# Performance work log

Hardware: AMD Instinct MI355X
Metric: run time of the kernel (lower is better)

Reference implementation:

```python
import jax, jax.numpy as jnp
import numpy as np

H = 12          # num_heads
HS = 64         # head_size
ALL = H * HS    # all_size = 768
P = 128         # max_position_offset


def _rel_pos_ids(S, P):
    # Toeplitz relative-position ids, same as scipy.linalg.toeplitz(c, r)
    r = np.clip(np.arange(S), None, P - 1)
    c = np.clip(-np.arange(S), -P + 1, None)
    c[1:] += 2 * P
    d = np.arange(S)[None, :] - np.arange(S)[:, None]  # j - i
    ids = np.where(d >= 0, r[np.clip(d, 0, None)], c[np.clip(-d, 0, None)])
    return jnp.asarray(ids, jnp.int32)


def setup_inputs() -> dict:
    key = jax.random.key(0)
    ks = jax.random.split(key, 8)
    B, S = 2, 1024
    return {
        "p0": jax.random.normal(ks[0], (1, 1), jnp.float32),
        "p1": jax.random.normal(ks[1], (B, S, ALL), jnp.float32),
        "p2": jax.random.normal(ks[2], (1, 1), jnp.float32),
        "W_qk": jax.random.normal(ks[3], (ALL, 2 * ALL), jnp.float32) * 0.02,
        "b_qk": jnp.zeros((2 * ALL,), jnp.float32),
        "rel_emb": jax.random.normal(ks[4], (2 * P + 2, HS), jnp.float32) * 0.02,
        "W_out": jax.random.normal(ks[5], (H, 64), jnp.float32) * 0.1,
        "b_out": jnp.zeros((64,), jnp.float32),
    }


def reference(p0, p1, p2, W_qk, b_qk, rel_emb, W_out, b_out):
    B, S, _ = p1.shape
    scaling = HS ** 0.25  # sqrt(sqrt(head_size))
    # reader[1]: Linear -> concat(query, key)
    u = p1 @ W_qk + b_qk                                        # [B,S,2*ALL]
    q = (u[..., :ALL] / scaling).reshape(B, S, H, HS).transpose(0, 2, 1, 3)  # [B,H,S,HS]
    k = (u[..., ALL:] / scaling).reshape(B, S, H, HS).transpose(0, 2, 1, 3)  # [B,H,S,HS]
    scores = jnp.einsum('bhsd,bhtd->bhst', q, k)                # [B,H,S,S]
    # relative position bias: rpe[s,t,:] . q[b,h,s,:]
    ids = _rel_pos_ids(S, P)                                    # [S,S] int
    rpe = rel_emb[ids] / scaling                                # [S,S,HS]
    bias = jnp.einsum('std,bhsd->bhst', rpe, q)                 # [B,H,S,S]
    out = (scores + bias).transpose(0, 2, 3, 1)                 # [B,S,S,H]
    # writer: Linear(num_heads -> predicate_dims[2])
    return out @ W_out + b_out                                  # [B,S,S,64]
```

## Files before the change

kernel.cpp:

```cpp
#include <hip/hip_runtime.h>
#include <math.h>

#define SEQ   1024
#define BATCH 2
#define NH    12
#define ALLD  768
#define INVS  0.35355339059327373f

typedef __attribute__((ext_vector_type(8)))  __bf16 bf16x8;
typedef __attribute__((ext_vector_type(16))) float  f32x16;
typedef __attribute__((ext_vector_type(2)))  float  f32x2;

__global__ __launch_bounds__(256) void qk_gemm(
    const float* __restrict__ p1, const float* __restrict__ Wqk,
    const float* __restrict__ bqk, __bf16* __restrict__ qf,
    __bf16* __restrict__ kf) {
  const int tid = threadIdx.x;
  const int l = tid & 63, w = tid >> 6;
  const int l31 = l & 31, half = l >> 5;
  const int m0 = blockIdx.x * 64;
  const int mw = (w >> 1) * 32;
  const int nw = blockIdx.y * 64 + (w & 1) * 32;

  __shared__ __bf16 Af[8][66][8];

  f32x16 acc;
#pragma unroll
  for (int e = 0; e < 16; ++e) acc[e] = 0.f;

  const int arow = tid >> 2;
  const int aq = tid & 3;

  for (int kk = 0; kk < 768; kk += 64) {
    __syncthreads();
    {
      const float* ap = p1 + (size_t)(m0 + arow) * 768 + kk + aq * 16;
      float4 a0 = ((const float4*)ap)[0];
      float4 a1 = ((const float4*)ap)[1];
      float4 a2 = ((const float4*)ap)[2];
      float4 a3 = ((const float4*)ap)[3];
      bf16x8 f0, f1;
      f0[0] = (__bf16)a0.x; f0[1] = (__bf16)a0.y;
      f0[2] = (__bf16)a0.z; f0[3] = (__bf16)a0.w;
      f0[4] = (__bf16)a1.x; f0[5] = (__bf16)a1.y;
      f0[6] = (__bf16)a1.z; f0[7] = (__bf16)a1.w;
      f1[0] = (__bf16)a2.x; f1[1] = (__bf16)a2.y;
      f1[2] = (__bf16)a2.z; f1[3] = (__bf16)a2.w;
      f1[4] = (__bf16)a3.x; f1[5] = (__bf16)a3.y;
      f1[6] = (__bf16)a3.z; f1[7] = (__bf16)a3.w;
      *(bf16x8*)&Af[aq * 2 + 0][arow][0] = f0;
      *(bf16x8*)&Af[aq * 2 + 1][arow][0] = f1;
    }
    __syncthreads();
#pragma unroll
    for (int ksl = 0; ksl < 4; ++ksl) {
      const float* bsrc =
          Wqk + (size_t)(kk + ksl * 16 + half * 8) * 1536 + nw + l31;
      bf16x8 bf;
#pragma unroll
      for (int e = 0; e < 8; ++e) bf[e] = (__bf16)bsrc[(size_t)e * 1536];
      bf16x8 af = *(const bf16x8*)&Af[ksl * 2 + half][mw + l31][0];
      acc = __builtin_amdgcn_mfma_f32_32x32x16_bf16(af, bf, acc, 0, 0, 0);
    }
  }

  const int n = nw + l31;
  const float bias = bqk[n];
  const bool is_q = (n < ALLD);
  const int nn = is_q ? n : n - ALLD;
  const int h = nn >> 6, dd = nn & 63;
  const int ks4 = dd >> 4, hf = (dd >> 3) & 1, e = dd & 7;
  __bf16* fdst = is_q ? qf : kf;
#pragma unroll
  for (int r = 0; r < 16; ++r) {
    const int m = m0 + mw + (r & 3) + 8 * (r >> 2) + 4 * half;
    const int bb = m >> 10, ss = m & 1023;
    const float v = (acc[r] + bias) * INVS;
    fdst[((((size_t)(bb * NH + h) * 4 + ks4) * 2 + hf) * SEQ + ss) * 8 + e] =
        (__bf16)v;
  }
}

__global__ __launch_bounds__(256, 4) void main_kernel(
    const __bf16* __restrict__ qf, const __bf16* __restrict__ kf,
    const float* __restrict__ rel, const float* __restrict__ Wout,
    const float* __restrict__ bout, float* __restrict__ out) {
  const int tid = threadIdx.x;
  const int l = tid & 63, w = tid >> 6;
  const int l31 = l & 31, half = l >> 5;

  const int raw = blockIdx.x + (blockIdx.y << 5) + (blockIdx.z << 10);
  const int swz = (raw & 7) * 256 + (raw >> 3);
  const int t0 = (swz & 31) * 32;
  const int s0 = ((swz >> 5) & 31) * 32;
  const int b = swz >> 10;
  const int D = t0 - s0;

  __shared__ __attribute__((aligned(16))) char smem[40960];
  float(*rel_s)[66] = (float(*)[66])smem;
  __bf16(*P)[20] = (__bf16(*)[20])smem;

  {
    const int c = tid >> 2, q = tid & 3;
    const int d = D - 32 + c;
    const int id = (d >= 0) ? (d < 127 ? d : 127) : (d > -127 ? d + 256 : 129);
    const float4* src = (const float4*)(rel + (size_t)id * 64 + q * 16);
    float4* dst = (float4*)&rel_s[c][q * 16];
#pragma unroll
    for (int i = 0; i < 4; ++i) dst[i] = src[i];
  }
  __syncthreads();

  bf16x8 relfrag[4][2];
#pragma unroll
  for (int ks = 0; ks < 4; ++ks) {
#pragma unroll
    for (int cb = 0; cb < 2; ++cb) {
      const int c = cb * 32 + l31;
      const int base = ks * 16 + half * 8;
      float4 r0 = *(const float4*)&rel_s[c][base];
      float4 r1 = *(const float4*)&rel_s[c][base + 4];
      bf16x8 f;
      f[0] = (__bf16)r0.x; f[1] = (__bf16)r0.y;
      f[2] = (__bf16)r0.z; f[3] = (__bf16)r0.w;
      f[4] = (__bf16)r1.x; f[5] = (__bf16)r1.y;
      f[6] = (__bf16)r1.z; f[7] = (__bf16)r1.w;
      relfrag[ks][cb] = f;
    }
  }
  __syncthreads();

  {
    ushort4 z = {0, 0, 0, 0};
#pragma unroll
    for (int i = 0; i < 4; ++i) *(ushort4*)&P[tid * 4 + i][12] = z;
  }

  const bf16x8* qfp = (const bf16x8*)qf;
  const bf16x8* kfp = (const bf16x8*)kf;

#pragma unroll
  for (int hh = 0; hh < 3; ++hh) {
    const int h = w * 3 + hh;
    f32x16 acc, bacc0, bacc1;
#pragma unroll
    for (int e = 0; e < 16; ++e) { acc[e] = 0.f; bacc0[e] = 0.f; bacc1[e] = 0.f; }
#pragma unroll
    for (int ks = 0; ks < 4; ++ks) {
      const size_t pbase = (((size_t)(b * NH + h) * 4 + ks) * 2 + half) * SEQ;
      bf16x8 af = qfp[pbase + s0 + l31];
      bf16x8 bvk = kfp[pbase + t0 + l31];
      acc = __builtin_amdgcn_mfma_f32_32x32x16_bf16(af, bvk, acc, 0, 0, 0);
      bacc0 = __builtin_amdgcn_mfma_f32_32x32x16_bf16(af, relfrag[ks][0],
                                                      bacc0, 0, 0, 0);
      bacc1 = __builtin_amdgcn_mfma_f32_32x32x16_bf16(af, relfrag[ks][1],
                                                      bacc1, 0, 0, 0);
    }
#pragma unroll
    for (int r = 0; r < 16; ++r) {
      const int sl = (r & 3) + 8 * (r >> 2) + 4 * half;
      const int src = (l31 - sl) & 31;
      const float v0 = __shfl(bacc0[r], src, 32);
      const float v1 = __shfl(bacc1[r], src, 32);
      const float bias = (l31 >= sl) ? v1 : v0;
      const float v = acc[r] + bias * INVS;
      P[sl * 32 + l31][h] = (__bf16)v;
    }
  }
  __syncthreads();

  bf16x8 wfrag0, wfrag1;
#pragma unroll
  for (int e = 0; e < 8; ++e) {
    const int hh = half * 8 + e;
    wfrag0[e] = (__bf16)((hh < NH) ? Wout[hh * 64 + 2 * l31] : 0.f);
    wfrag1[e] = (__bf16)((hh < NH) ? Wout[hh * 64 + 2 * l31 + 1] : 0.f);
  }
  const float bo0 = bout[2 * l31];
  const float bo1 = bout[2 * l31 + 1];

  float* obase = out + ((((size_t)b << 10) + s0) << 10) * 64 + (size_t)t0 * 64;
#pragma unroll 1
  for (int rt = w; rt < 32; rt += 4) {
    bf16x8 af = *(const bf16x8*)&P[rt * 32 + l31][half * 8];
    f32x16 o0, o1;
#pragma unroll
    for (int e = 0; e < 16; ++e) { o0[e] = 0.f; o1[e] = 0.f; }
    o0 = __builtin_amdgcn_mfma_f32_32x32x16_bf16(af, wfrag0, o0, 0, 0, 0);
    o1 = __builtin_amdgcn_mfma_f32_32x32x16_bf16(af, wfrag1, o1, 0, 0, 0);
    float* orow = obase + ((size_t)rt << 16) + 2 * l31;
#pragma unroll
    for (int r = 0; r < 16; ++r) {
      const int tl = (r & 3) + 8 * (r >> 2) + 4 * half;
      f32x2 v;
      v.x = o0[r] + bo0;
      v.y = o1[r] + bo1;
      __builtin_nontemporal_store(v, (f32x2*)(orow + ((size_t)tl << 6)));
    }
  }
}

extern "C" void kernel_launch(void* const* d_in, const int* in_sizes, int n_in,
                              void* d_out, int out_size, void* d_ws,
                              size_t ws_size, hipStream_t stream) {
  const float* p1 = (const float*)d_in[1];
  const float* Wqk = (const float*)d_in[3];
  const float* bqk = (const float*)d_in[4];
  const float* rel = (const float*)d_in[5];
  const float* Wout = (const float*)d_in[6];
  const float* bout = (const float*)d_in[7];
  float* out = (float*)d_out;

  __bf16* qf = (__bf16*)d_ws;
  __bf16* kf = qf + 1572864;

  hipLaunchKernelGGL(qk_gemm, dim3(32, 24), dim3(256), 0, stream, p1, Wqk, bqk,
                     qf, kf);
  hipLaunchKernelGGL(main_kernel, dim3(SEQ / 32, SEQ / 32, BATCH), dim3(256),
                     0, stream, qf, kf, rel, Wout, bout, out);
}
```

Baseline: 134.7 us.

## Widen main kernel tile to 32x64 and reuse rel embeddings across two subtiles

Each block of the main kernel now covers 64 key positions (two 32-wide subtiles) instead of 32, halving the grid to 1024 blocks. It loads 96 relative-embedding rows once, so the two subtiles share the middle 32-row fragment and reuse the Q fragments. It also drops the occupancy hint from the launch bounds. This is meant to amortise per-block setup (rel loads, bf16 conversion, W_out fragments). In exchange each block does more serial work, with an extra barrier between the subtiles, and holds more registers.

```diff
diff --git a/kernel.cpp b/kernel.cpp
--- a/kernel.cpp
+++ b/kernel.cpp
@@ -81,7 +81,7 @@
   }
 }
 
-__global__ __launch_bounds__(256, 4) void main_kernel(
+__global__ __launch_bounds__(256) void main_kernel(
     const __bf16* __restrict__ qf, const __bf16* __restrict__ kf,
     const float* __restrict__ rel, const float* __restrict__ Wout,
     const float* __restrict__ bout, float* __restrict__ out) {
@@ -89,33 +89,38 @@
   const int l = tid & 63, w = tid >> 6;
   const int l31 = l & 31, half = l >> 5;
 
-  const int raw = blockIdx.x + (blockIdx.y << 5) + (blockIdx.z << 10);
-  const int swz = (raw & 7) * 256 + (raw >> 3);
-  const int t0 = (swz & 31) * 32;
-  const int s0 = ((swz >> 5) & 31) * 32;
-  const int b = swz >> 10;
+  const int raw = blockIdx.x;
+  const int swz = (raw & 7) * 128 + (raw >> 3);
+  const int t0 = (swz & 15) * 64;
+  const int s0 = ((swz >> 4) & 31) * 32;
+  const int b = swz >> 9;
   const int D = t0 - s0;
 
   __shared__ __attribute__((aligned(16))) char smem[40960];
   float(*rel_s)[66] = (float(*)[66])smem;
   __bf16(*P)[20] = (__bf16(*)[20])smem;
 
-  {
-    const int c = tid >> 2, q = tid & 3;
-    const int d = D - 32 + c;
-    const int id = (d >= 0) ? (d < 127 ? d : 127) : (d > -127 ? d + 256 : 129);
-    const float4* src = (const float4*)(rel + (size_t)id * 64 + q * 16);
-    float4* dst = (float4*)&rel_s[c][q * 16];
-#pragma unroll
-    for (int i = 0; i < 4; ++i) dst[i] = src[i];
+#pragma unroll
+  for (int i = 0; i < 2; ++i) {
+    const int task = tid + 256 * i;
+    if (task < 384) {
+      const int c = task >> 2, q = task & 3;
+      const int d = D - 32 + c;
+      const int id =
+          (d >= 0) ? (d < 127 ? d : 127) : (d > -127 ? d + 256 : 129);
+      const float4* src = (const float4*)(rel + (size_t)id * 64 + q * 16);
+      float4* dst = (float4*)&rel_s[c][q * 16];
+#pragma unroll
+      for (int k = 0; k < 4; ++k) dst[k] = src[k];
+    }
   }
   __syncthreads();
 
-  bf16x8 relfrag[4][2];
+  bf16x8 relfrag[4][3];
 #pragma unroll
   for (int ks = 0; ks < 4; ++ks) {
 #pragma unroll
-    for (int cb = 0; cb < 2; ++cb) {
+    for (int cb = 0; cb < 3; ++cb) {
       const int c = cb * 32 + l31;
       const int base = ks * 16 + half * 8;
       float4 r0 = *(const float4*)&rel_s[c][base];
@@ -136,39 +141,6 @@
     for (int i = 0; i < 4; ++i) *(ushort4*)&P[tid * 4 + i][12] = z;
   }
 
-  const bf16x8* qfp = (const bf16x8*)qf;
-  const bf16x8* kfp = (const bf16x8*)kf;
-
-#pragma unroll
-  for (int hh = 0; hh < 3; ++hh) {
-    const int h = w * 3 + hh;
-    f32x16 acc, bacc0, bacc1;
-#pragma unroll
-    for (int e = 0; e < 16; ++e) { acc[e] = 0.f; bacc0[e] = 0.f; bacc1[e] = 0.f; }
-#pragma unroll
-    for (int ks = 0; ks < 4; ++ks) {
-      const size_t pbase = (((size_t)(b * NH + h) * 4 + ks) * 2 + half) * SEQ;
-      bf16x8 af = qfp[pbase + s0 + l31];
-      bf16x8 bvk = kfp[pbase + t0 + l31];
-      acc = __builtin_amdgcn_mfma_f32_32x32x16_bf16(af, bvk, acc, 0, 0, 0);
-      bacc0 = __builtin_amdgcn_mfma_f32_32x32x16_bf16(af, relfrag[ks][0],
-                                                      bacc0, 0, 0, 0);
-      bacc1 = __builtin_amdgcn_mfma_f32_32x32x16_bf16(af, relfrag[ks][1],
-                                                      bacc1, 0, 0, 0);
-    }
-#pragma unroll
-    for (int r = 0; r < 16; ++r) {
-      const int sl = (r & 3) + 8 * (r >> 2) + 4 * half;
-      const int src = (l31 - sl) & 31;
-      const float v0 = __shfl(bacc0[r], src, 32);
-      const float v1 = __shfl(bacc1[r], src, 32);
-      const float bias = (l31 >= sl) ? v1 : v0;
-      const float v = acc[r] + bias * INVS;
-      P[sl * 32 + l31][h] = (__bf16)v;
-    }
-  }
-  __syncthreads();
-
   bf16x8 wfrag0, wfrag1;
 #pragma unroll
   for (int e = 0; e < 8; ++e) {
@@ -179,24 +151,67 @@
   const float bo0 = bout[2 * l31];
   const float bo1 = bout[2 * l31 + 1];
 
-  float* obase = out + ((((size_t)b << 10) + s0) << 10) * 64 + (size_t)t0 * 64;
+  const bf16x8* qfp = (const bf16x8*)qf;
+  const bf16x8* kfp = (const bf16x8*)kf;
+
 #pragma unroll 1
-  for (int rt = w; rt < 32; rt += 4) {
-    bf16x8 af = *(const bf16x8*)&P[rt * 32 + l31][half * 8];
-    f32x16 o0, o1;
-#pragma unroll
-    for (int e = 0; e < 16; ++e) { o0[e] = 0.f; o1[e] = 0.f; }
-    o0 = __builtin_amdgcn_mfma_f32_32x32x16_bf16(af, wfrag0, o0, 0, 0, 0);
-    o1 = __builtin_amdgcn_mfma_f32_32x32x16_bf16(af, wfrag1, o1, 0, 0, 0);
-    float* orow = obase + ((size_t)rt << 16) + 2 * l31;
-#pragma unroll
-    for (int r = 0; r < 16; ++r) {
-      const int tl = (r & 3) + 8 * (r >> 2) + 4 * half;
-      f32x2 v;
-      v.x = o0[r] + bo0;
-      v.y = o1[r] + bo1;
-      __builtin_nontemporal_store(v, (f32x2*)(orow + ((size_t)tl << 6)));
-    }
+  for (int tt = 0; tt < 2; ++tt) {
+    const int tb = t0 + tt * 32;
+
+#pragma unroll
+    for (int hh = 0; hh < 3; ++hh) {
+      const int h = w * 3 + hh;
+      f32x16 acc, bacc0, bacc1;
+#pragma unroll
+      for (int e = 0; e < 16; ++e) {
+        acc[e] = 0.f; bacc0[e] = 0.f; bacc1[e] = 0.f;
+      }
+#pragma unroll
+      for (int ks = 0; ks < 4; ++ks) {
+        const size_t pbase =
+            (((size_t)(b * NH + h) * 4 + ks) * 2 + half) * SEQ;
+        bf16x8 af = qfp[pbase + s0 + l31];
+        bf16x8 bvk = kfp[pbase + tb + l31];
+        acc = __builtin_amdgcn_mfma_f32_32x32x16_bf16(af, bvk, acc, 0, 0, 0);
+        bacc0 = __builtin_amdgcn_mfma_f32_32x32x16_bf16(af, relfrag[ks][tt],
+                                                        bacc0, 0, 0, 0);
+        bacc1 = __builtin_amdgcn_mfma_f32_32x32x16_bf16(
+            af, relfrag[ks][tt + 1], bacc1, 0, 0, 0);
+      }
+#pragma unroll
+      for (int r = 0; r < 16; ++r) {
+        const int sl = (r & 3) + 8 * (r >> 2) + 4 * half;
+        const int src = (l31 - sl) & 31;
+        const float v0 = __shfl(bacc0[r], src, 32);
+        const float v1 = __shfl(bacc1[r], src, 32);
+        const float bias = (l31 >= sl) ? v1 : v0;
+        const float v = acc[r] + bias * INVS;
+        P[sl * 32 + l31][h] = (__bf16)v;
+      }
+    }
+    __syncthreads();
+
+    float* obase =
+        out + ((((size_t)b << 10) + s0) << 10) * 64 + (size_t)tb * 64;
+#pragma unroll 1
+    for (int rt = w; rt < 32; rt += 4) {
+      bf16x8 af = *(const bf16x8*)&P[rt * 32 + l31][half * 8];
+      f32x16 o0, o1;
+#pragma unroll
+      for (int e = 0; e < 16; ++e) { o0[e] = 0.f; o1[e] = 0.f; }
+      o0 = __builtin_amdgcn_mfma_f32_32x32x16_bf16(af, wfrag0, o0, 0, 0, 0);
+      o1 = __builtin_amdgcn_mfma_f32_32x32x16_bf16(af, wfrag1, o1, 0, 0, 0);
+      float* orow = obase + ((size_t)rt << 16) + 2 * l31;
+#pragma unroll
+      for (int r = 0; r < 16; ++r) {
+        const int tl = (r & 3) + 8 * (r >> 2) + 4 * half;
+        f32x2 v;
+        v.x = o0[r] + bo0;
+        v.y = o1[r] + bo1;
+        __builtin_nontemporal_store(v, (f32x2*)(orow + ((size_t)tl << 6)));
+      }
+    }
+    if (tt == 0) __syncthreads();
   }
 }
 
@@ -216,6 +231,6 @@
 
   hipLaunchKernelGGL(qk_gemm, dim3(32, 24), dim3(256), 0, stream, p1, Wqk, bqk,
                      qf, kf);
-  hipLaunchKernelGGL(main_kernel, dim3(SEQ / 32, SEQ / 32, BATCH), dim3(256),
-                     0, stream, qf, kf, rel, Wout, bout, out);
+  hipLaunchKernelGGL(main_kernel, dim3(1024), dim3(256), 0, stream, qf, kf,
+                     rel, Wout, bout, out);
 }
```

Measured after the change: 148.4 us. +10.2%, slower.
